# Performance work log

Hardware: AMD Instinct MI355X
Metric: run time of the kernel (lower is better)

## Reference

```python
import jax, jax.numpy as jnp
import numpy as np

N_NODES = 50000
N_EDGES = 1600000
IN_SIZE = 128
NUM_HEADS = 4
OUT_SIZE = 32


def setup_inputs() -> dict:
    key = jax.random.key(0)
    k1, k2, k3, k4 = jax.random.split(key, 4)
    feat = jax.random.normal(k1, (N_NODES, IN_SIZE), dtype=jnp.float32)
    src = jax.random.randint(k2, (N_EDGES,), 0, N_NODES)
    dst = jnp.sort(jax.random.randint(k3, (N_EDGES,), 0, N_NODES))
    # fc weight of DGL DotGatConv: Linear(in_size, num_heads*out_size, bias=False)
    W = jax.random.normal(k4, (IN_SIZE, NUM_HEADS * OUT_SIZE), dtype=jnp.float32) * 0.05
    return {"feat": feat, "src": src, "dst": dst, "W": W}


def reference(feat, src, dst, W):
    N = feat.shape[0]
    H, D = NUM_HEADS, OUT_SIZE
    # project: [N, H, D]
    h = (feat @ W).reshape(N, H, D)
    h_src = h[src]            # [E, H, D] gather
    h_dst = h[dst]            # [E, H, D] gather
    # per-edge dot-product attention score, scaled by sqrt(out_size)
    e = jnp.sum(h_src * h_dst, axis=-1) / jnp.sqrt(jnp.asarray(D, h.dtype))  # [E, H]
    # edge softmax over incoming edges of each destination node
    m = jax.ops.segment_max(e, dst, num_segments=N)        # [N, H]
    ex = jnp.exp(e - m[dst])                               # [E, H]
    s = jax.ops.segment_sum(ex, dst, num_segments=N)       # [N, H]
    alpha = ex / s[dst]                                    # [E, H]
    # weighted aggregation of source features: sum_e alpha_e * h_src_e -> dst
    out = jax.ops.segment_sum(alpha[:, :, None] * h_src, dst, num_segments=N)  # [N, H, D]
    return out
```

## Files before the change

kernel.cpp:

```cpp
#include <hip/hip_runtime.h>
#include <math.h>

#define N_NODES 50000
#define N_EDGES 1600000
#define IN_SIZE 128
#define HD 128
#define NUM_HEADS 4
#define OUT_SIZE 32
#define STRIPS (N_NODES / 16)
#define STRIPS_PER_WAVE 3
#define PROJ_WAVES ((STRIPS + STRIPS_PER_WAVE - 1) / STRIPS_PER_WAVE)
#define PROJ_BLOCKS ((PROJ_WAVES + 3) / 4)
#define OFF_BLOCKS ((N_NODES + 1 + 255) / 256)

#define SCALE2 0.25503486f

typedef _Float16 half8 __attribute__((ext_vector_type(8)));
typedef _Float16 half2v __attribute__((ext_vector_type(2)));
typedef __attribute__((ext_vector_type(4))) float floatx4;

static __device__ __forceinline__ half2v pk_f16(float a, float b) {
#if __has_builtin(__builtin_amdgcn_cvt_pkrtz)
    auto r = __builtin_amdgcn_cvt_pkrtz(a, b);
    union { decltype(r) i; half2v o; } u;
    u.i = r;
    return u.o;
#else
    half2v r; r.x = (_Float16)a; r.y = (_Float16)b; return r;
#endif
}

static __device__ __forceinline__ float dot2(half2v a, half2v b, float c) {
#if __has_builtin(__builtin_amdgcn_fdot2)
    return __builtin_amdgcn_fdot2(a, b, c, false);
#else
    return fmaf((float)a.x, (float)b.x, fmaf((float)a.y, (float)b.y, c));
#endif
}

__global__ __launch_bounds__(256, 1) void k_pre(const float* __restrict__ feat,
                                                const float* __restrict__ W,
                                                const int* __restrict__ dst,
                                                _Float16* __restrict__ hb,
                                                int* __restrict__ off) {
    if (blockIdx.x >= PROJ_BLOCKS) {
        int i = (blockIdx.x - PROJ_BLOCKS) * 256 + threadIdx.x;
        if (i <= N_NODES) {
            int lo = 0, hi = N_EDGES;
            while (lo < hi) {
                int mid = (lo + hi) >> 1;
                if (dst[mid] < i) lo = mid + 1; else hi = mid;
            }
            off[i] = lo;
        }
        return;
    }

    int wid = blockIdx.x * 4 + (threadIdx.x >> 6);
    int lane = threadIdx.x & 63;
    int s0 = wid * STRIPS_PER_WAVE;
    if (s0 >= STRIPS) return;
    int quad = lane >> 4;
    int l15 = lane & 15;

    half8 Bf[8][4];
#pragma unroll
    for (int t = 0; t < 8; t++) {
#pragma unroll
        for (int kb = 0; kb < 4; kb++) {
            union { half8 v; half2v h[4]; } bu;
#pragma unroll
            for (int jj = 0; jj < 4; jj++) {
                int k0 = kb * 32 + quad * 8 + 2 * jj;
                float lo = W[(size_t)k0 * HD + t * 16 + l15];
                float hi = W[(size_t)(k0 + 1) * HD + t * 16 + l15];
                bu.h[jj] = pk_f16(lo, hi);
            }
            Bf[t][kb] = bu.v;
        }
    }

    for (int it = 0; it < STRIPS_PER_WAVE; it++) {
        int strip = s0 + it;
        if (strip >= STRIPS) break;
        int row = strip * 16 + l15;

        const float* ab = feat + (size_t)row * IN_SIZE + quad * 8;
        float4 a[8];
#pragma unroll
        for (int kb = 0; kb < 4; kb++) {
            a[2 * kb]     = *(const float4*)(ab + kb * 32);
            a[2 * kb + 1] = *(const float4*)(ab + kb * 32 + 4);
        }

        floatx4 acc[8];
#pragma unroll
        for (int t = 0; t < 8; t++) acc[t] = (floatx4)(0.f);

#pragma unroll
        for (int kb = 0; kb < 4; kb++) {
            float4 x = a[2 * kb], y = a[2 * kb + 1];
            union { half8 v; half2v h[4]; } af;
            af.h[0] = pk_f16(x.x, x.y);
            af.h[1] = pk_f16(x.z, x.w);
            af.h[2] = pk_f16(y.x, y.y);
            af.h[3] = pk_f16(y.z, y.w);
#pragma unroll
            for (int t = 0; t < 8; t++)
                acc[t] = __builtin_amdgcn_mfma_f32_16x16x32_f16(af.v, Bf[t][kb], acc[t], 0, 0, 0);
        }

#pragma unroll
        for (int t = 0; t < 8; t++) {
#pragma unroll
            for (int r = 0; r < 4; r++) {
                int R = strip * 16 + quad * 4 + r;
                hb[(size_t)R * HD + t * 16 + l15] = (_Float16)acc[t][r];
            }
        }
    }
}

__global__ __launch_bounds__(256) void k_edge(const _Float16* __restrict__ hb,
                                              const int* __restrict__ src,
                                              const int* __restrict__ off,
                                              float* __restrict__ out) {
    int n = (blockIdx.x * 256 + threadIdx.x) >> 6;
    int lane = threadIdx.x & 63;
    if (n >= N_NODES) return;
    int e0 = off[n], e1 = off[n + 1];

    int g = lane >> 4;
    int p = lane & 15;

    const uint4* h4 = (const uint4*)hb;
    union U { uint4 v; half2v h[4]; };

    U hdv; hdv.v = h4[(size_t)n * 16 + p];
    half2v hdc[4];
    half2v sc2 = pk_f16(SCALE2, SCALE2);
#pragma unroll
    for (int d = 0; d < 4; d++) hdc[d] = hdv.h[d] * sc2;

    float s = 0.f;
    half2v acc2[4];
#pragma unroll
    for (int d = 0; d < 4; d++) acc2[d] = (half2v)(_Float16)0.f;

    int iters = (e1 - e0 + 3) >> 2;
    int nloop = (iters + 1) >> 1;

    int ea = e0 + g;
    bool aa = (ea < e1);
    int sa = aa ? src[ea] : n;
    U va; va.v = h4[(size_t)sa * 16 + p];

    int eb = ea + 4;
    bool ab = (eb < e1);
    int sb = ab ? src[eb] : n;
    U vb; vb.v = h4[(size_t)sb * 16 + p];

    for (int it = 0; it < nloop; it++) {
        int ec = ea + 8;
        bool ac = (ec < e1);
        int scn = ac ? src[ec] : n;
        U vc; vc.v = h4[(size_t)scn * 16 + p];

        int ed = eb + 8;
        bool ad = (ed < e1);
        int sdn = ad ? src[ed] : n;
        U vd; vd.v = h4[(size_t)sdn * 16 + p];

        {
            float p0 = dot2(va.h[0], hdc[0], 0.f);
            float p1 = dot2(va.h[1], hdc[1], 0.f);
            p0 = dot2(va.h[2], hdc[2], p0);
            p1 = dot2(va.h[3], hdc[3], p1);
            float pd = p0 + p1;
            pd += __shfl_xor(pd, 1);
            pd += __shfl_xor(pd, 2);
            float w = aa ? __builtin_amdgcn_exp2f(pd) : 0.f;
            s += w;
            half2v wh = pk_f16(w, w);
#pragma unroll
            for (int d = 0; d < 4; d++) acc2[d] += va.h[d] * wh;
        }
        {
            float p0 = dot2(vb.h[0], hdc[0], 0.f);
            float p1 = dot2(vb.h[1], hdc[1], 0.f);
            p0 = dot2(vb.h[2], hdc[2], p0);
            p1 = dot2(vb.h[3], hdc[3], p1);
            float pd = p0 + p1;
            pd += __shfl_xor(pd, 1);
            pd += __shfl_xor(pd, 2);
            float w = ab ? __builtin_amdgcn_exp2f(pd) : 0.f;
            s += w;
            half2v wh = pk_f16(w, w);
#pragma unroll
            for (int d = 0; d < 4; d++) acc2[d] += vb.h[d] * wh;
        }

        va = vc; aa = ac; ea = ec;
        vb = vd; ab = ad; eb = ed;
    }

    union B { half2v h; int i; };
#pragma unroll
    for (int d = 16; d <= 32; d <<= 1) {
        s += __shfl_xor(s, d);
#pragma unroll
        for (int j = 0; j < 4; j++) {
            B b; b.h = acc2[j];
            b.i = __shfl_xor(b.i, d);
            acc2[j] += b.h;
        }
    }

    if (g == 0) {
        float inv = (s > 0.f) ? 1.f / s : 0.f;
        float4 o0, o1;
        o0.x = (float)acc2[0].x * inv; o0.y = (float)acc2[0].y * inv;
        o0.z = (float)acc2[1].x * inv; o0.w = (float)acc2[1].y * inv;
        o1.x = (float)acc2[2].x * inv; o1.y = (float)acc2[2].y * inv;
        o1.z = (float)acc2[3].x * inv; o1.w = (float)acc2[3].y * inv;
        float4* op = (float4*)(out + (size_t)n * HD + 8 * p);
        op[0] = o0;
        op[1] = o1;
    }
}

extern "C" void kernel_launch(void* const* d_in, const int* in_sizes, int n_in,
                              void* d_out, int out_size, void* d_ws, size_t ws_size,
                              hipStream_t stream) {
    const float* feat = (const float*)d_in[0];
    const int*   src  = (const int*)d_in[1];
    const int*   dst  = (const int*)d_in[2];
    const float* W    = (const float*)d_in[3];
    float* out = (float*)d_out;

    char* ws = (char*)d_ws;
    _Float16* hb = (_Float16*)ws;
    int* off = (int*)(ws + (size_t)N_NODES * HD * 2);

    k_pre<<<PROJ_BLOCKS + OFF_BLOCKS, 256, 0, stream>>>(feat, W, dst, hb, off);
    k_edge<<<(N_NODES + 3) / 4, 256, 0, stream>>>(hb, src, off, out);
}
```

Measured before the change: 145.4 us.

## Stage W fragments in LDS for projection and deepen edge gather prefetch

The projection kernel now gives each wave a single 16-row strip. The fp16 W fragments are converted once per block into shared memory and read from there, instead of each wave building 32 register fragments from global memory and looping over three strips. This raises occupancy and parallelism for the projection. The edge kernel's software pipeline deepens from two to four in-flight gathered rows per lane group, to hide more gather latency. The cost is higher register pressure, a per-block W conversion plus a barrier, and a trip count rounded up to multiples of 16 edges, which can mean wasted iterations on low-degree nodes.

```diff
diff --git a/kernel.cpp b/kernel.cpp
--- a/kernel.cpp
+++ b/kernel.cpp
@@ -8,9 +8,7 @@
 #define NUM_HEADS 4
 #define OUT_SIZE 32
 #define STRIPS (N_NODES / 16)
-#define STRIPS_PER_WAVE 3
-#define PROJ_WAVES ((STRIPS + STRIPS_PER_WAVE - 1) / STRIPS_PER_WAVE)
-#define PROJ_BLOCKS ((PROJ_WAVES + 3) / 4)
+#define PROJ_BLOCKS ((STRIPS + 3) / 4)
 #define OFF_BLOCKS ((N_NODES + 1 + 255) / 256)
 
 #define SCALE2 0.25503486f
@@ -38,11 +36,11 @@
 #endif
 }
 
-__global__ __launch_bounds__(256, 1) void k_pre(const float* __restrict__ feat,
-                                                const float* __restrict__ W,
-                                                const int* __restrict__ dst,
-                                                _Float16* __restrict__ hb,
-                                                int* __restrict__ off) {
+__global__ __launch_bounds__(256) void k_pre(const float* __restrict__ feat,
+                                             const float* __restrict__ W,
+                                             const int* __restrict__ dst,
+                                             _Float16* __restrict__ hb,
+                                             int* __restrict__ off) {
     if (blockIdx.x >= PROJ_BLOCKS) {
         int i = (blockIdx.x - PROJ_BLOCKS) * 256 + threadIdx.x;
         if (i <= N_NODES) {
@@ -56,67 +54,68 @@
         return;
     }
 
-    int wid = blockIdx.x * 4 + (threadIdx.x >> 6);
-    int lane = threadIdx.x & 63;
-    int s0 = wid * STRIPS_PER_WAVE;
-    if (s0 >= STRIPS) return;
-    int quad = lane >> 4;
-    int l15 = lane & 15;
-
-    half8 Bf[8][4];
+    __shared__ _Float16 WF[32 * 64 * 8];
+
+    int tid = threadIdx.x;
+#pragma unroll
+    for (int i = 0; i < 8; i++) {
+        int entry = tid + 256 * i;
+        int fl = entry & 63;
+        int fi = entry >> 6;
+        int t = fi >> 2, kb = fi & 3;
+        int fq = fl >> 4, fl15 = fl & 15;
+        int c = t * 16 + fl15;
+        int k0 = kb * 32 + fq * 8;
+        union { half8 v; half2v h[4]; } bu;
+#pragma unroll
+        for (int j = 0; j < 4; j++) {
+            float lo = W[(size_t)(k0 + 2 * j) * HD + c];
+            float hi = W[(size_t)(k0 + 2 * j + 1) * HD + c];
+            bu.h[j] = pk_f16(lo, hi);
+        }
+        *(half8*)&WF[entry * 8] = bu.v;
+    }
+    __syncthreads();
+
+    int wave = tid >> 6, lane = tid & 63;
+    int strip = blockIdx.x * 4 + wave;
+    if (strip >= STRIPS) return;
+    int quad = lane >> 4, l15 = lane & 15;
+    int row = strip * 16 + l15;
+
+    const float* abp = feat + (size_t)row * IN_SIZE + quad * 8;
+    float4 a[8];
+#pragma unroll
+    for (int kb = 0; kb < 4; kb++) {
+        a[2 * kb]     = *(const float4*)(abp + kb * 32);
+        a[2 * kb + 1] = *(const float4*)(abp + kb * 32 + 4);
+    }
+
+    floatx4 acc[8];
+#pragma unroll
+    for (int t = 0; t < 8; t++) acc[t] = (floatx4)(0.f);
+
+#pragma unroll
+    for (int kb = 0; kb < 4; kb++) {
+        float4 x = a[2 * kb], y = a[2 * kb + 1];
+        union { half8 v; half2v h[4]; } af;
+        af.h[0] = pk_f16(x.x, x.y);
+        af.h[1] = pk_f16(x.z, x.w);
+        af.h[2] = pk_f16(y.x, y.y);
+        af.h[3] = pk_f16(y.z, y.w);
+#pragma unroll
+        for (int t = 0; t < 8; t++) {
+            half8 bf = *(const half8*)&WF[(size_t)((t * 4 + kb) * 64 + lane) * 8];
+            acc[t] = __builtin_amdgcn_mfma_f32_16x16x32_f16(af.v, bf, acc[t], 0, 0, 0);
+        }
+    }
+
 #pragma unroll
     for (int t = 0; t < 8; t++) {
 #pragma unroll
-        for (int kb = 0; kb < 4; kb++) {
-            union { half8 v; half2v h[4]; } bu;
-#pragma unroll
-            for (int jj = 0; jj < 4; jj++) {
-                int k0 = kb * 32 + quad * 8 + 2 * jj;
-                float lo = W[(size_t)k0 * HD + t * 16 + l15];
-                float hi = W[(size_t)(k0 + 1) * HD + t * 16 + l15];
-                bu.h[jj] = pk_f16(lo, hi);
-            }
-            Bf[t][kb] = bu.v;
-        }
-    }
-
-    for (int it = 0; it < STRIPS_PER_WAVE; it++) {
-        int strip = s0 + it;
-        if (strip >= STRIPS) break;
-        int row = strip * 16 + l15;
-
-        const float* ab = feat + (size_t)row * IN_SIZE + quad * 8;
-        float4 a[8];
-#pragma unroll
-        for (int kb = 0; kb < 4; kb++) {
-            a[2 * kb]     = *(const float4*)(ab + kb * 32);
-            a[2 * kb + 1] = *(const float4*)(ab + kb * 32 + 4);
-        }
-
-        floatx4 acc[8];
-#pragma unroll
-        for (int t = 0; t < 8; t++) acc[t] = (floatx4)(0.f);
-
-#pragma unroll
-        for (int kb = 0; kb < 4; kb++) {
-            float4 x = a[2 * kb], y = a[2 * kb + 1];
-            union { half8 v; half2v h[4]; } af;
-            af.h[0] = pk_f16(x.x, x.y);
-            af.h[1] = pk_f16(x.z, x.w);
-            af.h[2] = pk_f16(y.x, y.y);
-            af.h[3] = pk_f16(y.z, y.w);
-#pragma unroll
-            for (int t = 0; t < 8; t++)
-                acc[t] = __builtin_amdgcn_mfma_f32_16x16x32_f16(af.v, Bf[t][kb], acc[t], 0, 0, 0);
-        }
-
-#pragma unroll
-        for (int t = 0; t < 8; t++) {
-#pragma unroll
-            for (int r = 0; r < 4; r++) {
-                int R = strip * 16 + quad * 4 + r;
-                hb[(size_t)R * HD + t * 16 + l15] = (_Float16)acc[t][r];
-            }
+        for (int r = 0; r < 4; r++) {
+            int R = strip * 16 + quad * 4 + r;
+            hb[(size_t)R * HD + t * 16 + l15] = (_Float16)acc[t][r];
         }
     }
 }
@@ -148,60 +147,42 @@
     for (int d = 0; d < 4; d++) acc2[d] = (half2v)(_Float16)0.f;
 
     int iters = (e1 - e0 + 3) >> 2;
-    int nloop = (iters + 1) >> 1;
-
-    int ea = e0 + g;
-    bool aa = (ea < e1);
-    int sa = aa ? src[ea] : n;
-    U va; va.v = h4[(size_t)sa * 16 + p];
-
-    int eb = ea + 4;
-    bool ab = (eb < e1);
-    int sb = ab ? src[eb] : n;
-    U vb; vb.v = h4[(size_t)sb * 16 + p];
-
-    for (int it = 0; it < nloop; it++) {
-        int ec = ea + 8;
-        bool ac = (ec < e1);
-        int scn = ac ? src[ec] : n;
-        U vc; vc.v = h4[(size_t)scn * 16 + p];
-
-        int ed = eb + 8;
-        bool ad = (ed < e1);
-        int sdn = ad ? src[ed] : n;
-        U vd; vd.v = h4[(size_t)sdn * 16 + p];
-
-        {
-            float p0 = dot2(va.h[0], hdc[0], 0.f);
-            float p1 = dot2(va.h[1], hdc[1], 0.f);
-            p0 = dot2(va.h[2], hdc[2], p0);
-            p1 = dot2(va.h[3], hdc[3], p1);
+    int ntrip = (iters + 3) >> 2;
+
+    int ecur = e0 + g;
+    U buf[4]; bool ba[4];
+#pragma unroll
+    for (int j = 0; j < 4; j++) {
+        int ej = ecur + 4 * j;
+        ba[j] = (ej < e1);
+        int sj = ba[j] ? src[ej] : n;
+        buf[j].v = h4[(size_t)sj * 16 + p];
+    }
+
+    for (int it = 0; it < ntrip; it++) {
+#pragma unroll
+        for (int j = 0; j < 4; j++) {
+            int ep = ecur + 16;
+            bool ap = (ep < e1);
+            int sp = ap ? src[ep] : n;
+            U nb; nb.v = h4[(size_t)sp * 16 + p];
+
+            float p0 = dot2(buf[j].h[0], hdc[0], 0.f);
+            float p1 = dot2(buf[j].h[1], hdc[1], 0.f);
+            p0 = dot2(buf[j].h[2], hdc[2], p0);
+            p1 = dot2(buf[j].h[3], hdc[3], p1);
             float pd = p0 + p1;
             pd += __shfl_xor(pd, 1);
             pd += __shfl_xor(pd, 2);
-            float w = aa ? __builtin_amdgcn_exp2f(pd) : 0.f;
+            float w = ba[j] ? __builtin_amdgcn_exp2f(pd) : 0.f;
             s += w;
             half2v wh = pk_f16(w, w);
 #pragma unroll
-            for (int d = 0; d < 4; d++) acc2[d] += va.h[d] * wh;
-        }
-        {
-            float p0 = dot2(vb.h[0], hdc[0], 0.f);
-            float p1 = dot2(vb.h[1], hdc[1], 0.f);
-            p0 = dot2(vb.h[2], hdc[2], p0);
-            p1 = dot2(vb.h[3], hdc[3], p1);
-            float pd = p0 + p1;
-            pd += __shfl_xor(pd, 1);
-            pd += __shfl_xor(pd, 2);
-            float w = ab ? __builtin_amdgcn_exp2f(pd) : 0.f;
-            s += w;
-            half2v wh = pk_f16(w, w);
-#pragma unroll
-            for (int d = 0; d < 4; d++) acc2[d] += vb.h[d] * wh;
-        }
-
-        va = vc; aa = ac; ea = ec;
-        vb = vd; ab = ad; eb = ed;
+            for (int d = 0; d < 4; d++) acc2[d] += buf[j].h[d] * wh;
+
+            buf[j] = nb; ba[j] = ap;
+            ecur += 4;
+        }
     }
 
     union B { half2v h; int i; };
```

Result: slower. 149.1 us (+2.5%).
